# Kernel optimization log

Measured on AMD Instinct MI355X. Metric: run time of the kernel, lower is better.

Reference implementation:

```python
import jax, jax.numpy as jnp
import numpy as np


def setup_inputs() -> dict:
    key = jax.random.key(0)
    k1, k2, k3, k4 = jax.random.split(key, 4)
    N, E, F_IN, H, C = 100000, 1600000, 128, 64, 64
    x = jax.random.normal(k1, (N, F_IN), dtype=jnp.float32)
    edge_index = jax.random.randint(k2, (2, E), 0, N, dtype=jnp.int64)
    W1 = jax.random.normal(k3, (F_IN, H), dtype=jnp.float32) / np.sqrt(F_IN)
    b1 = jnp.zeros((H,), dtype=jnp.float32)
    W2 = jax.random.normal(k4, (H, C), dtype=jnp.float32) / np.sqrt(H)
    b2 = jnp.zeros((C,), dtype=jnp.float32)
    return {"x": x, "edge_index": edge_index, "W1": W1, "b1": b1, "W2": W2, "b2": b2}


def reference(x, edge_index, W1, b1, W2, b2):
    N = x.shape[0]
    # add self-loops (PyG GCNConv default)
    loop = jnp.arange(N, dtype=edge_index.dtype)
    src = jnp.concatenate([edge_index[0], loop])
    dst = jnp.concatenate([edge_index[1], loop])
    # symmetric normalization: deg^{-1/2}[src] * deg^{-1/2}[dst], deg over dst
    deg = jax.ops.segment_sum(jnp.ones_like(dst, dtype=x.dtype), dst, num_segments=N)
    dis = jnp.where(deg > 0, jax.lax.rsqrt(deg), 0.0)
    norm = dis[src] * dis[dst]  # [E+N]

    def gcn_conv(h, W, b):
        h = h @ W                                   # [N, out]
        msg = h[src] * norm[:, None]                # [E+N, out] gather
        agg = jax.ops.segment_sum(msg, dst, num_segments=N)  # scatter-add
        return agg + b

    h = jax.nn.relu(gcn_conv(x, W1, b1))
    # dropout inactive in eval mode
    out = gcn_conv(h, W2, b2)
    return jax.nn.log_softmax(out, axis=1)
```

## Files before the change

### kernel.cpp

```cpp
#include <hip/hip_runtime.h>
#include <cstdint>
#include <cstddef>

#define PASSA_EDGES 2048

typedef __attribute__((ext_vector_type(8))) short bf16x8;
typedef __attribute__((ext_vector_type(4))) float f32x4;


__device__ __forceinline__ unsigned short f2bf(float f) {
    unsigned int u = __float_as_uint(f);
    u += 0x7FFFu + ((u >> 16) & 1u);
    return (unsigned short)(u >> 16);
}
__device__ __forceinline__ float bf2f(unsigned short h) {
    return __uint_as_float((unsigned int)h << 16);
}

__device__ __forceinline__ void bf8_acc(uint4 u, float* acc) {
    acc[0] += __uint_as_float(u.x << 16);
    acc[1] += __uint_as_float(u.x & 0xFFFF0000u);
    acc[2] += __uint_as_float(u.y << 16);
    acc[3] += __uint_as_float(u.y & 0xFFFF0000u);
    acc[4] += __uint_as_float(u.z << 16);
    acc[5] += __uint_as_float(u.z & 0xFFFF0000u);
    acc[6] += __uint_as_float(u.w << 16);
    acc[7] += __uint_as_float(u.w & 0xFFFF0000u);
}
__device__ __forceinline__ void bf8_unpack(uint4 u, float* v) {
    v[0] = __uint_as_float(u.x << 16);
    v[1] = __uint_as_float(u.x & 0xFFFF0000u);
    v[2] = __uint_as_float(u.y << 16);
    v[3] = __uint_as_float(u.y & 0xFFFF0000u);
    v[4] = __uint_as_float(u.z << 16);
    v[5] = __uint_as_float(u.z & 0xFFFF0000u);
    v[6] = __uint_as_float(u.w << 16);
    v[7] = __uint_as_float(u.w & 0xFFFF0000u);
}


__global__ __launch_bounds__(256) void passA(const int* __restrict__ src,
                                             const int* __restrict__ dst,
                                             int* __restrict__ bcur,
                                             int2* __restrict__ bbuf, int E,
                                             int CAP, int shift) {
    __shared__ int2 bins[PASSA_EDGES];
    __shared__ int  cnt[256], off[256], cur[256], gbase[256];
    const int t  = threadIdx.x;
    const int e0 = blockIdx.x * PASSA_EDGES;
    const int n  = min(PASSA_EDGES, E - e0);

    cnt[t] = 0;
    __syncthreads();
    for (int i = t; i < n; i += 256) atomicAdd(&cnt[dst[e0 + i] >> shift], 1);
    __syncthreads();

    const int v = cnt[t];
    off[t] = v;
    __syncthreads();
    for (int o = 1; o < 256; o <<= 1) {
        int u = (t >= o) ? off[t - o] : 0;
        __syncthreads();
        off[t] += u;
        __syncthreads();
    }
    const int excl = off[t] - v;
    off[t] = excl;
    cur[t] = excl;
    if (v > 0) gbase[t] = t * CAP + atomicAdd(&bcur[t], v);
    __syncthreads();

    for (int i = t; i < n; i += 256) {
        const int d = dst[e0 + i];
        const int s = src[e0 + i];
        const int p = atomicAdd(&cur[d >> shift], 1);
        bins[p] = make_int2(s, d);
    }
    __syncthreads();

    for (int i = t; i < n; i += 256) {
        const int2 pr = bins[i];
        const int  b  = pr.y >> shift;
        const int  q  = gbase[b] + (i - off[b]);
        if (q < (b + 1) * CAP) bbuf[q] = pr;
    }
}


__global__ __launch_bounds__(256) void build_csr(const int2* __restrict__ bbuf,
                                                 const int* __restrict__ bcur,
                                                 int2* __restrict__ rowptr,
                                                 float* __restrict__ dis,
                                                 int* __restrict__ csr,
                                                 int N, int CAP, int CAPC, int shift) {
    __shared__ int cnt[1024];
    __shared__ int lcur[1024];
    __shared__ int psum[256];
    const int t     = threadIdx.x;
    const int b     = blockIdx.x;
    const int node0 = b << shift;
    const int nn    = min(1 << shift, N - node0);

    for (int j = t; j < nn; j += 256) cnt[j] = 0;
    __syncthreads();

    const int start = b * CAP;
    const int end   = min(b * CAP + bcur[b], (b + 1) * CAP);
    for (int e = start + t; e < end; e += 256)
        atomicAdd(&cnt[bbuf[e].y - node0], 1);
    __syncthreads();

    int v[4];
    int s = 0;
#pragma unroll
    for (int i = 0; i < 4; i++) {
        const int j = t * 4 + i;
        v[i] = (j < nn) ? ((cnt[j] + 7) & ~7) : 0;
        s += v[i];
    }
    psum[t] = s;
    __syncthreads();
    for (int o = 1; o < 256; o <<= 1) {
        int u = (t >= o) ? psum[t - o] : 0;
        __syncthreads();
        psum[t] += u;
        __syncthreads();
    }
    int run = b * CAPC + psum[t] - s;
#pragma unroll
    for (int i = 0; i < 4; i++) {
        const int j = t * 4 + i;
        if (j < nn) {
            lcur[j] = run;
            rowptr[node0 + j] = make_int2(run, v[i] >> 3);
            dis[node0 + j]    = rsqrtf((float)(cnt[j] + 1));
            run += v[i];
        }
    }
    __syncthreads();

    for (int e = start + t; e < end; e += 256) {
        const int2 pr = bbuf[e];
        const int  p  = atomicAdd(&lcur[pr.y - node0], 1);
        csr[p] = pr.x;
    }
    __syncthreads();

    int base2 = b * CAPC + psum[t] - s;
#pragma unroll
    for (int i = 0; i < 4; i++) {
        const int j = t * 4 + i;
        if (j < nn) {
            const int rowend = base2 + v[i];
            for (int p = lcur[j]; p < rowend; ++p) csr[p] = N;
            base2 += v[i];
        }
    }
}


__global__ __launch_bounds__(256) void prep_wfrag(const float* __restrict__ W1,
                                                  const float* __restrict__ W2,
                                                  unsigned short* __restrict__ whi1,
                                                  unsigned short* __restrict__ wlo1,
                                                  unsigned short* __restrict__ whi2,
                                                  unsigned short* __restrict__ wlo2) {
    for (int e = threadIdx.x; e < 128 * 64; e += 256) {
        const int blk = e >> 9, l = (e >> 3) & 63, j = e & 7;
        const int k = (blk >> 2) * 32 + (l >> 4) * 8 + j;
        const int n = (blk & 3) * 16 + (l & 15);
        const float v = W1[k * 64 + n];
        const unsigned short h = f2bf(v);
        whi1[e] = h;
        wlo1[e] = f2bf(v - bf2f(h));
    }
    for (int e = threadIdx.x; e < 64 * 64; e += 256) {
        const int blk = e >> 9, l = (e >> 3) & 63, j = e & 7;
        const int k = (blk >> 2) * 32 + (l >> 4) * 8 + j;
        const int n = (blk & 3) * 16 + (l & 15);
        const float v = W2[k * 64 + n];
        const unsigned short h = f2bf(v);
        whi2[e] = h;
        wlo2[e] = f2bf(v - bf2f(h));
    }
}


template <int K>
__global__ __launch_bounds__(256) void gemm_mfma(const float* __restrict__ X,
                                                 const unsigned short* __restrict__ whi,
                                                 const unsigned short* __restrict__ wlo,
                                                 const float* __restrict__ dis,
                                                 unsigned short* __restrict__ Yb, int N) {
    constexpr int LDX = K + 4;
    __shared__ float xs[64 * LDX];
    const int tid  = threadIdx.x;
    const int row0 = blockIdx.x * 64;

#pragma unroll
    for (int i = 0; i < (64 * K) / 1024; ++i) {
        const int fidx = i * 1024 + tid * 4;
        const int r = fidx / K, c = fidx % K;
        const float4 v = *(const float4*)(X + (size_t)min(row0 + r, N - 1) * K + c);
        *(float4*)&xs[r * LDX + c] = v;
    }
    __syncthreads();

    const int w = tid >> 6, l = tid & 63;
    const int m = l & 15, kg = l >> 4;

    f32x4 acc[4] = {};
    const float* xrow = &xs[(w * 16 + m) * LDX];

#pragma unroll
    for (int s = 0; s < K / 32; ++s) {
        const float4 a0 = *(const float4*)(xrow + s * 32 + kg * 8);
        const float4 a1 = *(const float4*)(xrow + s * 32 + kg * 8 + 4);
        const float av[8] = {a0.x, a0.y, a0.z, a0.w, a1.x, a1.y, a1.z, a1.w};
        bf16x8 ahi, alo;
#pragma unroll
        for (int j = 0; j < 8; ++j) {
            const unsigned short h = f2bf(av[j]);
            ahi[j] = (short)h;
            alo[j] = (short)f2bf(av[j] - bf2f(h));
        }
#pragma unroll
        for (int nt = 0; nt < 4; ++nt) {
            const bf16x8 bh = *(const bf16x8*)&whi[(s * 4 + nt) * 512 + l * 8];
            const bf16x8 bl = *(const bf16x8*)&wlo[(s * 4 + nt) * 512 + l * 8];
            acc[nt] = __builtin_amdgcn_mfma_f32_16x16x32_bf16(ahi, bh, acc[nt], 0, 0, 0);
            acc[nt] = __builtin_amdgcn_mfma_f32_16x16x32_bf16(alo, bh, acc[nt], 0, 0, 0);
            acc[nt] = __builtin_amdgcn_mfma_f32_16x16x32_bf16(ahi, bl, acc[nt], 0, 0, 0);
        }
    }

    float dv[4];
#pragma unroll
    for (int r = 0; r < 4; ++r)
        dv[r] = dis[min(row0 + w * 16 + kg * 4 + r, N - 1)];

#pragma unroll
    for (int nt = 0; nt < 4; ++nt)
#pragma unroll
        for (int r = 0; r < 4; ++r) {
            const int row = row0 + w * 16 + kg * 4 + r;
            if (row < N) Yb[(size_t)row * 64 + nt * 16 + m] = f2bf(acc[nt][r] * dv[r]);
        }
}


__device__ __forceinline__ void gather8i(const unsigned short* __restrict__ B,
                                         const int* __restrict__ csr,
                                         int s0, int iters, int co, float* acc) {
    const int4* cs = (const int4*)(csr + s0);
    int4 c0 = make_int4(0, 0, 0, 0), c1 = c0;
    if (iters > 0) { c0 = cs[0]; c1 = cs[1]; }
    for (int it = 0; it < iters; ++it) {
        const int nb = min(it + 1, iters - 1) * 2;
        int4 n0 = cs[nb], n1 = cs[nb + 1];
        uint4 u0 = *(const uint4*)&B[(size_t)c0.x * 64 + co * 8];
        uint4 u1 = *(const uint4*)&B[(size_t)c0.y * 64 + co * 8];
        uint4 u2 = *(const uint4*)&B[(size_t)c0.z * 64 + co * 8];
        uint4 u3 = *(const uint4*)&B[(size_t)c0.w * 64 + co * 8];
        uint4 u4 = *(const uint4*)&B[(size_t)c1.x * 64 + co * 8];
        uint4 u5 = *(const uint4*)&B[(size_t)c1.y * 64 + co * 8];
        uint4 u6 = *(const uint4*)&B[(size_t)c1.z * 64 + co * 8];
        uint4 u7 = *(const uint4*)&B[(size_t)c1.w * 64 + co * 8];
        bf8_acc(u0, acc);
        bf8_acc(u1, acc);
        bf8_acc(u2, acc);
        bf8_acc(u3, acc);
        bf8_acc(u4, acc);
        bf8_acc(u5, acc);
        bf8_acc(u6, acc);
        bf8_acc(u7, acc);
        c0 = n0; c1 = n1;
    }
}


__global__ __launch_bounds__(256) void agg_l1(const unsigned short* __restrict__ B,
                                              const int* __restrict__ csr,
                                              const int2* __restrict__ rowptr,
                                              const float* __restrict__ dis,
                                              const float* __restrict__ b1,
                                              float* __restrict__ hs, int N) {
    const int wid  = threadIdx.x >> 6;
    const int lane = threadIdx.x & 63;
    const int eg   = lane >> 3;
    const int co   = lane & 7;

    const int  row = blockIdx.x * 32 + wid * 8 + eg;
    const bool hr  = (row < N);

    const int2  rp = hr ? rowptr[row] : make_int2(0, 0);
    const float di = hr ? dis[row] : 0.f;

    float acc[8] = {};
    gather8i(B, csr, rp.x, rp.y, co, acc);

    if (!hr) return;

    uint4 us = *(const uint4*)&B[(size_t)row * 64 + co * 8];
    float bs[8];
    bf8_unpack(us, bs);
    float bb[8];
    *(float4*)&bb[0] = *(const float4*)&b1[co * 8];
    *(float4*)&bb[4] = *(const float4*)&b1[co * 8 + 4];

    float h[8];
#pragma unroll
    for (int i = 0; i < 8; i++)
        h[i] = fmaxf((acc[i] + bs[i]) * di + bb[i], 0.f);

    *(float4*)&hs[(size_t)row * 64 + co * 8]     = make_float4(h[0], h[1], h[2], h[3]);
    *(float4*)&hs[(size_t)row * 64 + co * 8 + 4] = make_float4(h[4], h[5], h[6], h[7]);
}


__global__ __launch_bounds__(256) void agg_l2(const unsigned short* __restrict__ B,
                                              const int* __restrict__ csr,
                                              const int2* __restrict__ rowptr,
                                              const float* __restrict__ dis,
                                              const float* __restrict__ b2,
                                              float* __restrict__ out, int N) {
    const int wid  = threadIdx.x >> 6;
    const int lane = threadIdx.x & 63;
    const int eg   = lane >> 3;
    const int co   = lane & 7;

    const int  row = blockIdx.x * 32 + wid * 8 + eg;
    const bool hr  = (row < N);

    const int2  rp = hr ? rowptr[row] : make_int2(0, 0);
    const float di = hr ? dis[row] : 0.f;

    float acc[8] = {};
    gather8i(B, csr, rp.x, rp.y, co, acc);

    if (!hr) return;

    uint4 us = *(const uint4*)&B[(size_t)row * 64 + co * 8];
    float bs[8];
    bf8_unpack(us, bs);
    float bb[8];
    *(float4*)&bb[0] = *(const float4*)&b2[co * 8];
    *(float4*)&bb[4] = *(const float4*)&b2[co * 8 + 4];

    float v[8];
#pragma unroll
    for (int i = 0; i < 8; i++) v[i] = (acc[i] + bs[i]) * di + bb[i];

    float m = v[0];
#pragma unroll
    for (int i = 1; i < 8; i++) m = fmaxf(m, v[i]);
#pragma unroll
    for (int off = 1; off <= 4; off <<= 1) m = fmaxf(m, __shfl_xor(m, off));
    float s = 0.f;
#pragma unroll
    for (int i = 0; i < 8; i++) s += __expf(v[i] - m);
#pragma unroll
    for (int off = 1; off <= 4; off <<= 1) s += __shfl_xor(s, off);
    float lse = m + __logf(s);

    float4 oa = make_float4(v[0] - lse, v[1] - lse, v[2] - lse, v[3] - lse);
    float4 ob = make_float4(v[4] - lse, v[5] - lse, v[6] - lse, v[7] - lse);
    *(float4*)&out[(size_t)row * 64 + co * 8]     = oa;
    *(float4*)&out[(size_t)row * 64 + co * 8 + 4] = ob;
}


extern "C" void kernel_launch(void* const* d_in, const int* in_sizes, int n_in,
                              void* d_out, int out_size, void* d_ws, size_t ws_size,
                              hipStream_t stream) {
    const float* x   = (const float*)d_in[0];
    const int*   ei  = (const int*)d_in[1];
    const float* W1  = (const float*)d_in[2];
    const float* b1  = (const float*)d_in[3];
    const float* W2  = (const float*)d_in[4];
    const float* b2  = (const float*)d_in[5];
    float*       out = (float*)d_out;

    const int  N   = in_sizes[0] / 128;
    const int  E   = in_sizes[1] / 2;
    const int* src = ei;
    const int* dst = ei + E;

    int shift = 9;
    while (((N - 1) >> shift) >= 256) shift++;
    const int NBUCK = ((N - 1) >> shift) + 1;
    const int CAP   = ((E / NBUCK) * 3 / 2 + 255) & ~255;
    const int CAPC  = CAP + 8 * (1 << shift);

    auto align256 = [](size_t v) { return (v + 255) & ~(size_t)255; };
    char*           p        = (char*)d_ws;
    float*          dis      = (float*)p;          p += align256((size_t)N * 4);
    int2*           rowptr   = (int2*)p;           p += align256((size_t)N * 8);
    int*            bcur     = (int*)p;            p += align256(256 * 4);
    int*            csr      = (int*)p;            p += align256((size_t)NBUCK * CAPC * 4);
    int2*           bbuf     = (int2*)p;           p += align256((size_t)NBUCK * CAP * 8);
    unsigned short* xwb      = (unsigned short*)p; p += align256((size_t)(N + 1) * 64 * 2);
    unsigned short* whi1     = (unsigned short*)p; p += align256(128 * 64 * 2);
    unsigned short* wlo1     = (unsigned short*)p; p += align256(128 * 64 * 2);
    unsigned short* whi2     = (unsigned short*)p; p += align256(64 * 64 * 2);
    unsigned short* wlo2     = (unsigned short*)p; p += align256(64 * 64 * 2);

    float* hs = out;

    hipMemsetAsync(bcur, 0, 256 * 4, stream);
    hipMemsetAsync(xwb + (size_t)N * 64, 0, 64 * 2, stream);
    prep_wfrag<<<1, 256, 0, stream>>>(W1, W2, whi1, wlo1, whi2, wlo2);
    passA<<<(E + PASSA_EDGES - 1) / PASSA_EDGES, 256, 0, stream>>>(src, dst, bcur, bbuf, E, CAP, shift);
    build_csr<<<NBUCK, 256, 0, stream>>>(bbuf, bcur, rowptr, dis, csr, N, CAP, CAPC, shift);

    gemm_mfma<128><<<(N + 63) / 64, 256, 0, stream>>>(x, whi1, wlo1, dis, xwb, N);
    agg_l1<<<(N + 31) / 32, 256, 0, stream>>>(xwb, csr, rowptr, dis, b1, hs, N);
    gemm_mfma<64><<<(N + 63) / 64, 256, 0, stream>>>(hs, whi2, wlo2, dis, xwb, N);
    agg_l2<<<(N + 31) / 32, 256, 0, stream>>>(xwb, csr, rowptr, dis, b2, out, N);
}
```

Before: 250.7 us.

## Fuse layer-2 GEMM into layer-1 aggregation and fold memsets into prep kernel

The layer-1 aggregation kernel now stages its ReLU output for 32 rows in shared memory and immediately multiplies it by W2 with split-bf16 MFMA, scaling by dis and writing bf16 rows into a new h2b buffer. This removes the fp32 hidden-state round trip through global memory and one kernel launch. The two hipMemsetAsync calls are folded into the prep_wfrag kernel. The cost is extra shared memory and MFMA work inside a memory-bound gather kernel, plus a __syncthreads that may reduce overlap.

After: 236.6 us. 5.6% less time.

```diff
diff --git a/kernel.cpp b/kernel.cpp
--- a/kernel.cpp
+++ b/kernel.cpp
@@ -164,7 +164,16 @@
                                                   unsigned short* __restrict__ whi1,
                                                   unsigned short* __restrict__ wlo1,
                                                   unsigned short* __restrict__ whi2,
-                                                  unsigned short* __restrict__ wlo2) {
+                                                  unsigned short* __restrict__ wlo2,
+                                                  int* __restrict__ bcur,
+                                                  unsigned short* __restrict__ xwb,
+                                                  unsigned short* __restrict__ h2b,
+                                                  int N) {
+    bcur[threadIdx.x] = 0;
+    if (threadIdx.x < 64) {
+        xwb[(size_t)N * 64 + threadIdx.x] = 0;
+        h2b[(size_t)N * 64 + threadIdx.x] = 0;
+    }
     for (int e = threadIdx.x; e < 128 * 64; e += 256) {
         const int blk = e >> 9, l = (e >> 3) & 63, j = e & 7;
         const int k = (blk >> 2) * 32 + (l >> 4) * 8 + j;
@@ -279,18 +288,23 @@
 }
 
 
-__global__ __launch_bounds__(256) void agg_l1(const unsigned short* __restrict__ B,
-                                              const int* __restrict__ csr,
-                                              const int2* __restrict__ rowptr,
-                                              const float* __restrict__ dis,
-                                              const float* __restrict__ b1,
-                                              float* __restrict__ hs, int N) {
+__global__ __launch_bounds__(256) void agg_l1f(const unsigned short* __restrict__ B,
+                                               const int* __restrict__ csr,
+                                               const int2* __restrict__ rowptr,
+                                               const float* __restrict__ dis,
+                                               const float* __restrict__ b1,
+                                               const unsigned short* __restrict__ whi2,
+                                               const unsigned short* __restrict__ wlo2,
+                                               unsigned short* __restrict__ h2b, int N) {
+    __shared__ float hsm[32][68];
+    __shared__ float dsm[32];
     const int wid  = threadIdx.x >> 6;
     const int lane = threadIdx.x & 63;
     const int eg   = lane >> 3;
     const int co   = lane & 7;
-
-    const int  row = blockIdx.x * 32 + wid * 8 + eg;
+    const int lrow = wid * 8 + eg;
+
+    const int  row = blockIdx.x * 32 + lrow;
     const bool hr  = (row < N);
 
     const int2  rp = hr ? rowptr[row] : make_int2(0, 0);
@@ -299,22 +313,63 @@
     float acc[8] = {};
     gather8i(B, csr, rp.x, rp.y, co, acc);
 
-    if (!hr) return;
-
-    uint4 us = *(const uint4*)&B[(size_t)row * 64 + co * 8];
-    float bs[8];
-    bf8_unpack(us, bs);
-    float bb[8];
-    *(float4*)&bb[0] = *(const float4*)&b1[co * 8];
-    *(float4*)&bb[4] = *(const float4*)&b1[co * 8 + 4];
-
-    float h[8];
-#pragma unroll
-    for (int i = 0; i < 8; i++)
-        h[i] = fmaxf((acc[i] + bs[i]) * di + bb[i], 0.f);
-
-    *(float4*)&hs[(size_t)row * 64 + co * 8]     = make_float4(h[0], h[1], h[2], h[3]);
-    *(float4*)&hs[(size_t)row * 64 + co * 8 + 4] = make_float4(h[4], h[5], h[6], h[7]);
+    float h[8] = {};
+    if (hr) {
+        uint4 us = *(const uint4*)&B[(size_t)row * 64 + co * 8];
+        float bs[8];
+        bf8_unpack(us, bs);
+        float bb[8];
+        *(float4*)&bb[0] = *(const float4*)&b1[co * 8];
+        *(float4*)&bb[4] = *(const float4*)&b1[co * 8 + 4];
+#pragma unroll
+        for (int i = 0; i < 8; i++)
+            h[i] = fmaxf((acc[i] + bs[i]) * di + bb[i], 0.f);
+    }
+    *(float4*)&hsm[lrow][co * 8]     = make_float4(h[0], h[1], h[2], h[3]);
+    *(float4*)&hsm[lrow][co * 8 + 4] = make_float4(h[4], h[5], h[6], h[7]);
+    if (co == 0) dsm[lrow] = di;
+    __syncthreads();
+
+    const int m  = lane & 15, kg = lane >> 4;
+    const int rt = wid & 1;
+    const int n0t = wid >> 1;
+
+    f32x4 o[2] = {};
+#pragma unroll
+    for (int s = 0; s < 2; ++s) {
+        const float* hrow = &hsm[rt * 16 + m][s * 32 + kg * 8];
+        float av[8];
+#pragma unroll
+        for (int j = 0; j < 8; ++j) av[j] = hrow[j];
+        bf16x8 ahi, alo;
+#pragma unroll
+        for (int j = 0; j < 8; ++j) {
+            const unsigned short hh = f2bf(av[j]);
+            ahi[j] = (short)hh;
+            alo[j] = (short)f2bf(av[j] - bf2f(hh));
+        }
+#pragma unroll
+        for (int p = 0; p < 2; ++p) {
+            const int nt = n0t + p * 2;
+            const bf16x8 bh = *(const bf16x8*)&whi2[(s * 4 + nt) * 512 + lane * 8];
+            const bf16x8 bl = *(const bf16x8*)&wlo2[(s * 4 + nt) * 512 + lane * 8];
+            o[p] = __builtin_amdgcn_mfma_f32_16x16x32_bf16(ahi, bh, o[p], 0, 0, 0);
+            o[p] = __builtin_amdgcn_mfma_f32_16x16x32_bf16(alo, bh, o[p], 0, 0, 0);
+            o[p] = __builtin_amdgcn_mfma_f32_16x16x32_bf16(ahi, bl, o[p], 0, 0, 0);
+        }
+    }
+
+#pragma unroll
+    for (int p = 0; p < 2; ++p) {
+        const int nt = n0t + p * 2;
+#pragma unroll
+        for (int r = 0; r < 4; ++r) {
+            const int lr   = rt * 16 + kg * 4 + r;
+            const int orow = blockIdx.x * 32 + lr;
+            if (orow < N)
+                h2b[(size_t)orow * 64 + nt * 16 + m] = f2bf(o[p][r] * dsm[lr]);
+        }
+    }
 }
 
 
@@ -400,21 +455,17 @@
     int*            csr      = (int*)p;            p += align256((size_t)NBUCK * CAPC * 4);
     int2*           bbuf     = (int2*)p;           p += align256((size_t)NBUCK * CAP * 8);
     unsigned short* xwb      = (unsigned short*)p; p += align256((size_t)(N + 1) * 64 * 2);
+    unsigned short* h2b      = (unsigned short*)p; p += align256((size_t)(N + 1) * 64 * 2);
     unsigned short* whi1     = (unsigned short*)p; p += align256(128 * 64 * 2);
     unsigned short* wlo1     = (unsigned short*)p; p += align256(128 * 64 * 2);
     unsigned short* whi2     = (unsigned short*)p; p += align256(64 * 64 * 2);
     unsigned short* wlo2     = (unsigned short*)p; p += align256(64 * 64 * 2);
 
-    float* hs = out;
-
-    hipMemsetAsync(bcur, 0, 256 * 4, stream);
-    hipMemsetAsync(xwb + (size_t)N * 64, 0, 64 * 2, stream);
-    prep_wfrag<<<1, 256, 0, stream>>>(W1, W2, whi1, wlo1, whi2, wlo2);
+    prep_wfrag<<<1, 256, 0, stream>>>(W1, W2, whi1, wlo1, whi2, wlo2, bcur, xwb, h2b, N);
     passA<<<(E + PASSA_EDGES - 1) / PASSA_EDGES, 256, 0, stream>>>(src, dst, bcur, bbuf, E, CAP, shift);
     build_csr<<<NBUCK, 256, 0, stream>>>(bbuf, bcur, rowptr, dis, csr, N, CAP, CAPC, shift);
 
     gemm_mfma<128><<<(N + 63) / 64, 256, 0, stream>>>(x, whi1, wlo1, dis, xwb, N);
-    agg_l1<<<(N + 31) / 32, 256, 0, stream>>>(xwb, csr, rowptr, dis, b1, hs, N);
-    gemm_mfma<64><<<(N + 63) / 64, 256, 0, stream>>>(hs, whi2, wlo2, dis, xwb, N);
-    agg_l2<<<(N + 31) / 32, 256, 0, stream>>>(xwb, csr, rowptr, dis, b2, out, N);
-}
+    agg_l1f<<<(N + 31) / 32, 256, 0, stream>>>(xwb, csr, rowptr, dis, b1, whi2, wlo2, h2b, N);
+    agg_l2<<<(N + 31) / 32, 256, 0, stream>>>(h2b, csr, rowptr, dis, b2, out, N);
+}
```
